# Kernel tuning notes

Measured on AMD Instinct MI355X. Metric: run time of the kernel, lower is better.

Reference implementation:

```python
import jax, jax.numpy as jnp
from jax import lax
import numpy as np


def setup_inputs() -> dict:
    key = jax.random.key(0)
    ks = jax.random.split(key, 5)
    B, T, I, H, L = 64, 512, 1024, 1024, 1
    stdv = 1.0 / (H ** 0.5)
    return {
        "input": jax.random.normal(ks[0], (B, T, I), dtype=jnp.float32),
        "weight_ih": jax.random.uniform(ks[1], (L, H, I), jnp.float32, -stdv, stdv),
        "weight_hh": jax.random.uniform(ks[2], (L, H, H), jnp.float32, -stdv, stdv),
        "bias_ih": jax.random.uniform(ks[3], (L, H), jnp.float32, -stdv, stdv),
        "bias_hh": jax.random.uniform(ks[4], (L, H), jnp.float32, -stdv, stdv),
    }


def reference(input, weight_ih, weight_hh, bias_ih, bias_hh):
    # input: (B, T, I); weights per layer; hx: (L, B, H)
    L, H, I = weight_ih.shape
    B, T, _ = input.shape
    h0 = jnp.zeros((L, B, H), dtype=input.dtype)
    bias = (bias_ih + bias_hh)[:, None, :]  # (L, 1, H)
    # Hoist the input projection out of the recurrence: one big GEMM.
    x_proj = jnp.einsum("bti,lhi->tlbh", input, weight_ih)  # (T, L, B, H)

    def step(h, xp):
        # h: (L, B, H); per-layer recurrent matmul
        g = xp + jnp.einsum("lbh,lgh->lbg", h, weight_hh) + bias
        h_new = jnp.tanh(g)
        return h_new, h_new

    h_last, outs = lax.scan(step, h0, x_proj)  # outs: (T, L, B, H)
    output = jnp.transpose(outs, (1, 0, 2, 3))  # (L, T, B, H) matching torch cat(dim=1)
    return output, h_last
```

## Files before the change

### kernel.cpp

```cpp
#include <hip/hip_runtime.h>
#include <hip/hip_bf16.h>
#include <stdint.h>

#define B_ 64
#define T_ 512
#define I_ 1024
#define H_ 1024
#define BH (B_*H_)

typedef __attribute__((ext_vector_type(8))) short short8;
typedef __attribute__((ext_vector_type(4))) float f32x4;
typedef __attribute__((ext_vector_type(4))) unsigned u32x4;
typedef __attribute__((ext_vector_type(2))) unsigned u32x2;

static __device__ __forceinline__ unsigned short f2bf(float f) {
  union { float f; unsigned u; } v; v.f = f;
  unsigned r = v.u + 0x7fffu + ((v.u >> 16) & 1u);
  return (unsigned short)(r >> 16);
}

static __device__ __forceinline__ void glds16(const void* g, void* l) {
  __builtin_amdgcn_global_load_lds(
      (const __attribute__((address_space(1))) unsigned int*)g,
      (__attribute__((address_space(3))) unsigned int*)l, 16, 0, 0);
}

__global__ void convert_weights(const f32x4* __restrict__ wih, const f32x4* __restrict__ whh,
                                uint2* __restrict__ wih_b, uint2* __restrict__ whh_b)
{
  int idx = blockIdx.x * blockDim.x + threadIdx.x;
  f32x4 a = wih[idx];
  uint2 o;
  o.x = f2bf(a[0]) | ((unsigned)f2bf(a[1]) << 16);
  o.y = f2bf(a[2]) | ((unsigned)f2bf(a[3]) << 16);
  wih_b[idx] = o;
  f32x4 b = whh[idx];
  uint2 p;
  p.x = f2bf(b[0]) | ((unsigned)f2bf(b[1]) << 16);
  p.y = f2bf(b[2]) | ((unsigned)f2bf(b[3]) << 16);
  whh_b[idx] = p;
}

__launch_bounds__(256)
__global__ void gemm_xproj(const float* __restrict__ in,
                           const unsigned short* __restrict__ wb,
                           const float* __restrict__ bih,
                           const float* __restrict__ bhh,
                           float* __restrict__ out)
{
  __shared__ __align__(16) unsigned char As[16384];
  __shared__ __align__(16) unsigned char Bs[16384];
  const int tid = threadIdx.x;
  const int lane = tid & 63;
  const int w = tid >> 6;
  const int wm = w >> 1, wn = w & 1;
  const int bn = blockIdx.x, bm = blockIdx.y;

  const int ar = tid >> 1;
  const int ah = tid & 1;
  const int R0 = bm*128 + ar;
  const float* asrc = in + (size_t)(R0 & 63) * (T_*I_) + (size_t)(R0 >> 6) * I_ + ah*32;
  unsigned char* adst_base = As + ar*128;
  const int aswz_w = (ar & 7) << 4;

  f32x4 acc[4][4];
  #pragma unroll
  for (int i = 0; i < 4; ++i)
    #pragma unroll
    for (int j = 0; j < 4; ++j)
      acc[i][j] = (f32x4){0.f,0.f,0.f,0.f};

  f32x4 av[8];
  #pragma unroll
  for (int j = 0; j < 8; ++j) av[j] = *(const f32x4*)(asrc + 0*64 + j*4);

  for (int kt = 0; kt < 16; ++kt) {
    __syncthreads();
    #pragma unroll
    for (int q = 0; q < 4; ++q) {
      int inst = w*4 + q;
      int rb = inst*8 + (lane >> 3);
      int srcoff = ((bn*128 + rb) * I_ + kt*64) * 2 + (((lane & 7) * 16) ^ ((rb & 7) << 4));
      glds16((const unsigned char*)wb + srcoff, Bs + inst*1024);
    }
    #pragma unroll
    for (int j2 = 0; j2 < 4; ++j2) {
      uint4 val;
      f32x4 v0 = av[j2*2], v1 = av[j2*2+1];
      val.x = f2bf(v0[0]) | ((unsigned)f2bf(v0[1]) << 16);
      val.y = f2bf(v0[2]) | ((unsigned)f2bf(v0[3]) << 16);
      val.z = f2bf(v1[0]) | ((unsigned)f2bf(v1[1]) << 16);
      val.w = f2bf(v1[2]) | ((unsigned)f2bf(v1[3]) << 16);
      int koffb = ah*64 + j2*16;
      *(uint4*)(adst_base + (koffb ^ aswz_w)) = val;
    }
    __syncthreads();
    if (kt < 15) {
      #pragma unroll
      for (int j = 0; j < 8; ++j) av[j] = *(const f32x4*)(asrc + (kt+1)*64 + j*4);
    }
    #pragma unroll
    for (int kb = 0; kb < 2; ++kb) {
      const int kby = kb*64 + ((lane >> 4) << 4);
      short8 af[4], bfr[4];
      #pragma unroll
      for (int i = 0; i < 4; ++i) {
        int ra = wm*64 + i*16 + (lane & 15);
        af[i] = *(const short8*)(As + ra*128 + (kby ^ ((ra & 7) << 4)));
      }
      #pragma unroll
      for (int j = 0; j < 4; ++j) {
        int rb2 = wn*64 + j*16 + (lane & 15);
        bfr[j] = *(const short8*)(Bs + rb2*128 + (kby ^ ((rb2 & 7) << 4)));
      }
      #pragma unroll
      for (int i = 0; i < 4; ++i)
        #pragma unroll
        for (int j = 0; j < 4; ++j)
          acc[i][j] = __builtin_amdgcn_mfma_f32_16x16x32_bf16(af[i], bfr[j], acc[i][j], 0, 0, 0);
    }
  }
  #pragma unroll
  for (int j = 0; j < 4; ++j) {
    int col = bn*128 + wn*64 + j*16 + (lane & 15);
    float bias = bih[col] + bhh[col];
    #pragma unroll
    for (int i = 0; i < 4; ++i) {
      int Rb = bm*128 + wm*64 + i*16 + ((lane >> 4) << 2);
      #pragma unroll
      for (int q = 0; q < 4; ++q) {
        int R = Rb + q;
        out[(size_t)(R >> 6) * BH + (size_t)(R & 63) * H_ + col] = acc[i][j][q] + bias;
      }
    }
  }
}

__launch_bounds__(256, 1)
__global__ void rnn_recur(const unsigned short* __restrict__ whh_b,
                          float* __restrict__ out,
                          unsigned char* __restrict__ hx)
{
  extern __shared__ __align__(16) unsigned char lds[];
  const int tid = threadIdx.x;
  const int lane = tid & 63;
  const int w = tid >> 6;
  const int g = blockIdx.x;
  const int gb = g >> 4;
  const int gn = g & 15;

  for (int q = 0; q < 32; ++q) {
    int inst = w*32 + q;
    int nl = inst >> 1;
    int koff = (inst & 1)*1024 + lane*16;
    size_t srcoff = (size_t)(gn*64 + nl)*2048 + (size_t)(koff ^ ((nl & 7) << 4));
    glds16((const unsigned char*)whh_b + srcoff, lds + inst*1024);
  }
  asm volatile("s_waitcnt vmcnt(0)" ::: "memory");
  __syncthreads();

  const int arow = w*16 + (lane & 15);
  const unsigned char* wsrow = lds + (size_t)arow*2048;
  const int aswz = (arow & 7) << 4;
  const int klane = (lane >> 4) << 4;
  short8 af[32];
  #pragma unroll
  for (int kb = 0; kb < 32; ++kb)
    af[kb] = *(const short8*)(wsrow + ((kb*64 + klane) ^ aswz));
  __syncthreads();

  const int bb = lane & 15;
  const int nq = (lane >> 4) << 2;
  const int colb = gn*64 + w*16 + nq;
  const int brow = gb*16 + bb;
  const int bswz = (bb & 7) << 4;

  const int srow = tid & 15;
  const int scol = tid >> 4;
  const int sswz = (srow & 7) << 4;

  f32x4 xp = *(const f32x4*)(out + (size_t)brow*H_ + colb);

  for (int t = 0; t < T_; ++t) {
    unsigned char* hsb = lds + (size_t)(t & 1)*32768;
    unsigned char* sdst = hsb + srow*2048;
    if (t == 0) {
      u32x2 z = (u32x2){0u, 0u};
      #pragma unroll
      for (int j = 0; j < 16; ++j)
        *(u32x2*)(sdst + (((j*16 + scol)*8) ^ sswz)) = z;
    } else {
      const unsigned want = (unsigned)t;
      const unsigned char* pb = hx + (size_t)(t & 1)*262144 + (size_t)gb*65536 + (size_t)tid*16;
      u32x4 v0,v1,v2,v3,v4,v5,v6,v7,v8,v9,v10,v11,v12,v13,v14,v15;
      for (;;) {
        asm volatile(
          "global_load_dwordx4 %0, %8, off sc0 sc1\n\t"
          "global_load_dwordx4 %1, %9, off sc0 sc1\n\t"
          "global_load_dwordx4 %2, %10, off sc0 sc1\n\t"
          "global_load_dwordx4 %3, %11, off sc0 sc1\n\t"
          "global_load_dwordx4 %4, %12, off sc0 sc1\n\t"
          "global_load_dwordx4 %5, %13, off sc0 sc1\n\t"
          "global_load_dwordx4 %6, %14, off sc0 sc1\n\t"
          "global_load_dwordx4 %7, %15, off sc0 sc1"
          : "=&v"(v0),"=&v"(v1),"=&v"(v2),"=&v"(v3),"=&v"(v4),"=&v"(v5),"=&v"(v6),"=&v"(v7)
          : "v"(pb), "v"(pb+4096), "v"(pb+2*4096), "v"(pb+3*4096),
            "v"(pb+4*4096), "v"(pb+5*4096), "v"(pb+6*4096), "v"(pb+7*4096)
          : "memory");
        asm volatile(
          "global_load_dwordx4 %0, %8, off sc0 sc1\n\t"
          "global_load_dwordx4 %1, %9, off sc0 sc1\n\t"
          "global_load_dwordx4 %2, %10, off sc0 sc1\n\t"
          "global_load_dwordx4 %3, %11, off sc0 sc1\n\t"
          "global_load_dwordx4 %4, %12, off sc0 sc1\n\t"
          "global_load_dwordx4 %5, %13, off sc0 sc1\n\t"
          "global_load_dwordx4 %6, %14, off sc0 sc1\n\t"
          "global_load_dwordx4 %7, %15, off sc0 sc1"
          : "=&v"(v8),"=&v"(v9),"=&v"(v10),"=&v"(v11),"=&v"(v12),"=&v"(v13),"=&v"(v14),"=&v"(v15)
          : "v"(pb+8*4096), "v"(pb+9*4096), "v"(pb+10*4096), "v"(pb+11*4096),
            "v"(pb+12*4096), "v"(pb+13*4096), "v"(pb+14*4096), "v"(pb+15*4096)
          : "memory");
        asm volatile("s_waitcnt vmcnt(0)"
          : "+v"(v0),"+v"(v1),"+v"(v2),"+v"(v3),"+v"(v4),"+v"(v5),"+v"(v6),"+v"(v7),
            "+v"(v8),"+v"(v9),"+v"(v10),"+v"(v11),"+v"(v12),"+v"(v13),"+v"(v14),"+v"(v15)
          :: "memory");
        int ok = 1;
        #define CHK(vv, jj) if ((jj) != gn && vv[2] != want) ok = 0;
        CHK(v0,0)  CHK(v1,1)  CHK(v2,2)  CHK(v3,3)
        CHK(v4,4)  CHK(v5,5)  CHK(v6,6)  CHK(v7,7)
        CHK(v8,8)  CHK(v9,9)  CHK(v10,10) CHK(v11,11)
        CHK(v12,12) CHK(v13,13) CHK(v14,14) CHK(v15,15)
        #undef CHK
        if (ok) break;
        __builtin_amdgcn_s_sleep(1);
      }
      #define STG(vv, jj) if ((jj) != gn) \
        *(u32x2*)(sdst + ((((jj)*16 + scol)*8) ^ sswz)) = (u32x2){vv[0], vv[1]};
      STG(v0,0)  STG(v1,1)  STG(v2,2)  STG(v3,3)
      STG(v4,4)  STG(v5,5)  STG(v6,6)  STG(v7,7)
      STG(v8,8)  STG(v9,9)  STG(v10,10) STG(v11,11)
      STG(v12,12) STG(v13,13) STG(v14,14) STG(v15,15)
      #undef STG
    }
    asm volatile("s_waitcnt lgkmcnt(0)\n\ts_barrier" ::: "memory");

    const unsigned char* hfrow = hsb + (size_t)bb*2048;
    f32x4 acc0 = (f32x4){0.f,0.f,0.f,0.f}, acc1 = (f32x4){0.f,0.f,0.f,0.f};
    #pragma unroll
    for (int kb = 0; kb < 32; kb += 2) {
      short8 b0 = *(const short8*)(hfrow + ((kb*64 + klane) ^ bswz));
      short8 b1 = *(const short8*)(hfrow + (((kb+1)*64 + klane) ^ bswz));
      acc0 = __builtin_amdgcn_mfma_f32_16x16x32_bf16(af[kb],   b0, acc0, 0, 0, 0);
      acc1 = __builtin_amdgcn_mfma_f32_16x16x32_bf16(af[kb+1], b1, acc1, 0, 0, 0);
    }
    f32x4 hval;
    #pragma unroll
    for (int q = 0; q < 4; ++q)
      hval[q] = tanhf(acc0[q] + acc1[q] + xp[q]);

    u32x4 pkt;
    pkt[0] = f2bf(hval[0]) | ((unsigned)f2bf(hval[1]) << 16);
    pkt[1] = f2bf(hval[2]) | ((unsigned)f2bf(hval[3]) << 16);
    pkt[2] = (unsigned)(t + 1);
    pkt[3] = 0u;
    const unsigned char* wp = hx + (size_t)((t+1) & 1)*262144 + (size_t)gb*65536
                              + (size_t)(gn*256 + tid)*16;
    asm volatile("global_store_dwordx4 %0, %1, off sc0 sc1" :: "v"(wp), "v"(pkt) : "memory");

    unsigned char* hsn = lds + (size_t)((t+1) & 1)*32768;
    *(u32x2*)(hsn + (size_t)bb*2048 + ((colb*2) ^ bswz)) = (u32x2){pkt[0], pkt[1]};

    *(f32x4*)(out + (size_t)t*BH + (size_t)brow*H_ + colb) = hval;
    if (t == T_-1)
      *(f32x4*)(out + (size_t)T_*BH + (size_t)brow*H_ + colb) = hval;

    int tn = (t < T_-1) ? t+1 : t;
    xp = *(const f32x4*)(out + (size_t)tn*BH + (size_t)brow*H_ + colb);
  }
}

extern "C" void kernel_launch(void* const* d_in, const int* in_sizes, int n_in,
                              void* d_out, int out_size, void* d_ws, size_t ws_size,
                              hipStream_t stream)
{
  const float* in  = (const float*)d_in[0];
  const float* wih = (const float*)d_in[1];
  const float* whh = (const float*)d_in[2];
  const float* bih = (const float*)d_in[3];
  const float* bhh = (const float*)d_in[4];
  float* out = (float*)d_out;
  unsigned char* ws = (unsigned char*)d_ws;

  unsigned char*  hx    = ws;
  unsigned short* wih_b = (unsigned short*)(ws + 524288);
  unsigned short* whh_b = (unsigned short*)(ws + 524288 + 2097152);

  hipMemsetAsync(hx, 0, 524288, stream);
  convert_weights<<<1024, 256, 0, stream>>>((const f32x4*)wih, (const f32x4*)whh,
                                            (uint2*)wih_b, (uint2*)whh_b);
  gemm_xproj<<<dim3(8, 256), 256, 0, stream>>>(in, wih_b, bih, bhh, out);
  rnn_recur<<<64, 256, 131072, stream>>>(whh_b, out, hx);
}
```

Measured before the change: 1.768 ms.

## Pin recurrence groups to XCDs via atomic ticket and use L2-local polling

```diff
diff --git a/kernel.cpp b/kernel.cpp
--- a/kernel.cpp
+++ b/kernel.cpp
@@ -142,12 +142,20 @@
                           unsigned char* __restrict__ hx)
 {
   extern __shared__ __align__(16) unsigned char lds[];
+  __shared__ unsigned stick;
+  unsigned xcc;
+  asm volatile("s_getreg_b32 %0, hwreg(HW_REG_XCC_ID)" : "=s"(xcc));
+  if (xcc >= 4) return;
+  if (threadIdx.x == 0)
+    stick = atomicAdd((unsigned*)(hx + 524288 + (size_t)xcc*4), 1u);
+  __syncthreads();
+  if (stick >= 16) return;
+  const int gb = (int)xcc;
+  const int gn = (int)stick;
+
   const int tid = threadIdx.x;
   const int lane = tid & 63;
   const int w = tid >> 6;
-  const int g = blockIdx.x;
-  const int gb = g >> 4;
-  const int gn = g & 15;
 
   for (int q = 0; q < 32; ++q) {
     int inst = w*32 + q;
@@ -193,33 +201,63 @@
       const unsigned want = (unsigned)t;
       const unsigned char* pb = hx + (size_t)(t & 1)*262144 + (size_t)gb*65536 + (size_t)tid*16;
       u32x4 v0,v1,v2,v3,v4,v5,v6,v7,v8,v9,v10,v11,v12,v13,v14,v15;
+      int rounds = 0;
       for (;;) {
-        asm volatile(
-          "global_load_dwordx4 %0, %8, off sc0 sc1\n\t"
-          "global_load_dwordx4 %1, %9, off sc0 sc1\n\t"
-          "global_load_dwordx4 %2, %10, off sc0 sc1\n\t"
-          "global_load_dwordx4 %3, %11, off sc0 sc1\n\t"
-          "global_load_dwordx4 %4, %12, off sc0 sc1\n\t"
-          "global_load_dwordx4 %5, %13, off sc0 sc1\n\t"
-          "global_load_dwordx4 %6, %14, off sc0 sc1\n\t"
-          "global_load_dwordx4 %7, %15, off sc0 sc1"
-          : "=&v"(v0),"=&v"(v1),"=&v"(v2),"=&v"(v3),"=&v"(v4),"=&v"(v5),"=&v"(v6),"=&v"(v7)
-          : "v"(pb), "v"(pb+4096), "v"(pb+2*4096), "v"(pb+3*4096),
-            "v"(pb+4*4096), "v"(pb+5*4096), "v"(pb+6*4096), "v"(pb+7*4096)
-          : "memory");
-        asm volatile(
-          "global_load_dwordx4 %0, %8, off sc0 sc1\n\t"
-          "global_load_dwordx4 %1, %9, off sc0 sc1\n\t"
-          "global_load_dwordx4 %2, %10, off sc0 sc1\n\t"
-          "global_load_dwordx4 %3, %11, off sc0 sc1\n\t"
-          "global_load_dwordx4 %4, %12, off sc0 sc1\n\t"
-          "global_load_dwordx4 %5, %13, off sc0 sc1\n\t"
-          "global_load_dwordx4 %6, %14, off sc0 sc1\n\t"
-          "global_load_dwordx4 %7, %15, off sc0 sc1"
-          : "=&v"(v8),"=&v"(v9),"=&v"(v10),"=&v"(v11),"=&v"(v12),"=&v"(v13),"=&v"(v14),"=&v"(v15)
-          : "v"(pb+8*4096), "v"(pb+9*4096), "v"(pb+10*4096), "v"(pb+11*4096),
-            "v"(pb+12*4096), "v"(pb+13*4096), "v"(pb+14*4096), "v"(pb+15*4096)
-          : "memory");
+        if (rounds < 6) {
+          asm volatile(
+            "global_load_dwordx4 %0, %8, off nt\n\t"
+            "global_load_dwordx4 %1, %9, off nt\n\t"
+            "global_load_dwordx4 %2, %10, off nt\n\t"
+            "global_load_dwordx4 %3, %11, off nt\n\t"
+            "global_load_dwordx4 %4, %12, off nt\n\t"
+            "global_load_dwordx4 %5, %13, off nt\n\t"
+            "global_load_dwordx4 %6, %14, off nt\n\t"
+            "global_load_dwordx4 %7, %15, off nt"
+            : "=&v"(v0),"=&v"(v1),"=&v"(v2),"=&v"(v3),"=&v"(v4),"=&v"(v5),"=&v"(v6),"=&v"(v7)
+            : "v"(pb), "v"(pb+4096), "v"(pb+2*4096), "v"(pb+3*4096),
+              "v"(pb+4*4096), "v"(pb+5*4096), "v"(pb+6*4096), "v"(pb+7*4096)
+            : "memory");
+          asm volatile(
+            "global_load_dwordx4 %0, %8, off nt\n\t"
+            "global_load_dwordx4 %1, %9, off nt\n\t"
+            "global_load_dwordx4 %2, %10, off nt\n\t"
+            "global_load_dwordx4 %3, %11, off nt\n\t"
+            "global_load_dwordx4 %4, %12, off nt\n\t"
+            "global_load_dwordx4 %5, %13, off nt\n\t"
+            "global_load_dwordx4 %6, %14, off nt\n\t"
+            "global_load_dwordx4 %7, %15, off nt"
+            : "=&v"(v8),"=&v"(v9),"=&v"(v10),"=&v"(v11),"=&v"(v12),"=&v"(v13),"=&v"(v14),"=&v"(v15)
+            : "v"(pb+8*4096), "v"(pb+9*4096), "v"(pb+10*4096), "v"(pb+11*4096),
+              "v"(pb+12*4096), "v"(pb+13*4096), "v"(pb+14*4096), "v"(pb+15*4096)
+            : "memory");
+        } else {
+          asm volatile(
+            "global_load_dwordx4 %0, %8, off sc0 sc1\n\t"
+            "global_load_dwordx4 %1, %9, off sc0 sc1\n\t"
+            "global_load_dwordx4 %2, %10, off sc0 sc1\n\t"
+            "global_load_dwordx4 %3, %11, off sc0 sc1\n\t"
+            "global_load_dwordx4 %4, %12, off sc0 sc1\n\t"
+            "global_load_dwordx4 %5, %13, off sc0 sc1\n\t"
+            "global_load_dwordx4 %6, %14, off sc0 sc1\n\t"
+            "global_load_dwordx4 %7, %15, off sc0 sc1"
+            : "=&v"(v0),"=&v"(v1),"=&v"(v2),"=&v"(v3),"=&v"(v4),"=&v"(v5),"=&v"(v6),"=&v"(v7)
+            : "v"(pb), "v"(pb+4096), "v"(pb+2*4096), "v"(pb+3*4096),
+              "v"(pb+4*4096), "v"(pb+5*4096), "v"(pb+6*4096), "v"(pb+7*4096)
+            : "memory");
+          asm volatile(
+            "global_load_dwordx4 %0, %8, off sc0 sc1\n\t"
+            "global_load_dwordx4 %1, %9, off sc0 sc1\n\t"
+            "global_load_dwordx4 %2, %10, off sc0 sc1\n\t"
+            "global_load_dwordx4 %3, %11, off sc0 sc1\n\t"
+            "global_load_dwordx4 %4, %12, off sc0 sc1\n\t"
+            "global_load_dwordx4 %5, %13, off sc0 sc1\n\t"
+            "global_load_dwordx4 %6, %14, off sc0 sc1\n\t"
+            "global_load_dwordx4 %7, %15, off sc0 sc1"
+            : "=&v"(v8),"=&v"(v9),"=&v"(v10),"=&v"(v11),"=&v"(v12),"=&v"(v13),"=&v"(v14),"=&v"(v15)
+            : "v"(pb+8*4096), "v"(pb+9*4096), "v"(pb+10*4096), "v"(pb+11*4096),
+              "v"(pb+12*4096), "v"(pb+13*4096), "v"(pb+14*4096), "v"(pb+15*4096)
+            : "memory");
+        }
         asm volatile("s_waitcnt vmcnt(0)"
           : "+v"(v0),"+v"(v1),"+v"(v2),"+v"(v3),"+v"(v4),"+v"(v5),"+v"(v6),"+v"(v7),
             "+v"(v8),"+v"(v9),"+v"(v10),"+v"(v11),"+v"(v12),"+v"(v13),"+v"(v14),"+v"(v15)
@@ -232,6 +270,7 @@
         CHK(v12,12) CHK(v13,13) CHK(v14,14) CHK(v15,15)
         #undef CHK
         if (ok) break;
+        ++rounds;
         __builtin_amdgcn_s_sleep(1);
       }
       #define STG(vv, jj) if ((jj) != gn) \
@@ -265,7 +304,9 @@
     pkt[3] = 0u;
     const unsigned char* wp = hx + (size_t)((t+1) & 1)*262144 + (size_t)gb*65536
                               + (size_t)(gn*256 + tid)*16;
-    asm volatile("global_store_dwordx4 %0, %1, off sc0 sc1" :: "v"(wp), "v"(pkt) : "memory");
+    asm volatile("global_store_dwordx4 %0, %1, off\n\t"
+                 "global_store_dwordx4 %0, %1, off sc0 sc1"
+                 :: "v"(wp), "v"(pkt) : "memory");
 
     unsigned char* hsn = lds + (size_t)((t+1) & 1)*32768;
     *(u32x2*)(hsn + (size_t)bb*2048 + ((colb*2) ^ bswz)) = (u32x2){pkt[0], pkt[1]};
@@ -276,6 +317,18 @@
 
     int tn = (t < T_-1) ? t+1 : t;
     xp = *(const f32x4*)(out + (size_t)tn*BH + (size_t)brow*H_ + colb);
+  }
+
+  {
+    u32x4 z4 = (u32x4){0u,0u,0u,0u};
+    const unsigned char* wp0 = hx + (size_t)gb*65536 + (size_t)(gn*256 + tid)*16;
+    const unsigned char* wp1 = wp0 + 262144;
+    asm volatile("global_store_dwordx4 %0, %2, off\n\t"
+                 "global_store_dwordx4 %0, %2, off sc0 sc1\n\t"
+                 "global_store_dwordx4 %1, %2, off\n\t"
+                 "global_store_dwordx4 %1, %2, off sc0 sc1\n\t"
+                 "s_waitcnt vmcnt(0)"
+                 :: "v"(wp0), "v"(wp1), "v"(z4) : "memory");
   }
 }
 
@@ -292,12 +345,12 @@
   unsigned char* ws = (unsigned char*)d_ws;
 
   unsigned char*  hx    = ws;
-  unsigned short* wih_b = (unsigned short*)(ws + 524288);
-  unsigned short* whh_b = (unsigned short*)(ws + 524288 + 2097152);
-
-  hipMemsetAsync(hx, 0, 524288, stream);
+  unsigned short* wih_b = (unsigned short*)(ws + 532480);
+  unsigned short* whh_b = (unsigned short*)(ws + 532480 + 2097152);
+
+  hipMemsetAsync(hx, 0, 532480, stream);
   convert_weights<<<1024, 256, 0, stream>>>((const f32x4*)wih, (const f32x4*)whh,
                                             (uint2*)wih_b, (uint2*)whh_b);
   gemm_xproj<<<dim3(8, 256), 256, 0, stream>>>(in, wih_b, bih, bhh, out);
-  rnn_recur<<<64, 256, 131072, stream>>>(whh_b, out, hx);
-}
+  rnn_recur<<<1024, 256, 131072, stream>>>(whh_b, out, hx);
+}
```

Result: slower. 2.128 ms (+20.3%).
